# Kernel tuning notes

Measured on AMD Instinct MI355X. Metric: run time of the kernel, lower is better.

## Reference

```python
import jax, jax.numpy as jnp
import numpy as np

B, N, D, P = 8, 256, 1024, 512  # batch, n_words, input_dim, proj_dim


def setup_inputs() -> dict:
    key = jax.random.key(0)
    ks = jax.random.split(key, 8)
    w = lambda k, shape: (jax.random.normal(k, shape, dtype=jnp.float32) * 0.02)
    return {
        "x": jax.random.normal(ks[0], (B, N, D), dtype=jnp.float32),
        # bigram path
        "Wl": w(ks[1], (P, D)), "bl": jnp.zeros((P,), jnp.float32),
        "Wr": w(ks[2], (P, D)),  # right proj has no bias
        "Wo": w(ks[3], (1, P)), "bo": jnp.zeros((1,), jnp.float32),
        # start builder: Linear -> ReLU -> Linear
        "Ws1": w(ks[4], (P, D)), "bs1": jnp.zeros((P,), jnp.float32),
        "Ws2": w(ks[5], (1, P)), "bs2": jnp.zeros((1,), jnp.float32),
        # end builder
        "We1": w(ks[6], (P, D)), "be1": jnp.zeros((P,), jnp.float32),
        "We2": w(ks[7], (1, P)), "be2": jnp.zeros((1,), jnp.float32),
    }


def reference(x, Wl, bl, Wr, Wo, bo, Ws1, bs1, Ws2, bs2, We1, be1, We2, be2):
    # start / end scorers: [B,N,1]
    start = jax.nn.relu(jnp.einsum('bnd,pd->bnp', x, Ws1) + bs1) @ Ws2.T + bs2
    end = jax.nn.relu(jnp.einsum('bnd,pd->bnp', x, We1) + be1) @ We2.T + be2
    # bigram projections: [B,N,P]
    left = jnp.einsum('bnd,pd->bnp', x, Wl) + bl
    right = jnp.einsum('bnd,pd->bnp', x, Wr)
    # outer-sum: proj[b,i,j,:] = left[b,j,:] + right[b,i,:]  -> [B,N,N,P]
    proj = jax.nn.relu(left[:, None, :, :] + right[:, :, None, :])
    bigram = jnp.einsum('bijp,qp->bijq', proj, Wo) + bo  # [B,N,N,1]
    return (bigram, start, end)
```

## Files before the change

### kernel.cpp

```cpp
#include <hip/hip_runtime.h>

typedef __attribute__((ext_vector_type(8))) short short8;
typedef __attribute__((ext_vector_type(4))) float f32x4;

constexpr int kB = 8;
constexpr int kN = 256;
constexpr int kD = 1024;
constexpr int kP = 512;
constexpr int kM = kB * kN;

__global__ __launch_bounds__(256) void cvt_kernel(
    const float* __restrict__ x,
    const float* __restrict__ Wl, const float* __restrict__ Wr,
    const float* __restrict__ Ws1, const float* __restrict__ We1,
    unsigned short* __restrict__ xb, unsigned short* __restrict__ wb)
{
    const int g = blockIdx.x * 256 + threadIdx.x;
    const float* src;
    unsigned short* dst;
    if (g < 262144) {
        src = x + (size_t)g * 8;
        dst = xb + (size_t)g * 8;
    } else {
        const int gg = g - 262144;
        const int w = gg >> 16;
        const int r = gg & 65535;
        const float* s = (w == 0) ? Wl : (w == 1) ? Wr : (w == 2) ? Ws1 : We1;
        src = s + (size_t)r * 8;
        dst = wb + ((size_t)w << 19) + (size_t)r * 8;
    }
    const float4 a = *reinterpret_cast<const float4*>(src);
    const float4 b = *reinterpret_cast<const float4*>(src + 4);
    const float v[8] = {a.x, a.y, a.z, a.w, b.x, b.y, b.z, b.w};
    short8 o;
#pragma unroll
    for (int i = 0; i < 8; ++i) {
        unsigned u = __float_as_uint(v[i]);
        u = u + 0x7FFF + ((u >> 16) & 1);
        o[i] = (short)(u >> 16);
    }
    *reinterpret_cast<short8*>(dst) = o;
}

__global__ __launch_bounds__(256) void proj_mfma(
    const unsigned short* __restrict__ xb, const unsigned short* __restrict__ wb,
    const float* __restrict__ bl, const float* __restrict__ bs1,
    const float* __restrict__ be1,
    float* __restrict__ left_t, float* __restrict__ right_t,
    float* __restrict__ hs, float* __restrict__ he)
{
    const int z = blockIdx.z;
    const unsigned short* W = wb + ((size_t)z << 19);
    const float* bias = (z == 0) ? bl : (z == 2) ? bs1 : (z == 3) ? be1 : nullptr;
    float* dst = (z == 0) ? left_t : (z == 1) ? right_t : (z == 2) ? hs : he;
    const bool relu = (z >= 2);
    const bool transp = (z < 2);

    __shared__ unsigned short As[128 * 32];
    __shared__ unsigned short Bs[64 * 32];

    const int r0 = blockIdx.x * 128;
    const int p0 = blockIdx.y * 64;
    const int t = threadIdx.x;
    const int wid = t >> 6;
    const int lane = t & 63;
    const int wr = wid >> 1;
    const int wc = wid & 1;

    f32x4 acc[4][2] = {};

    const int lrow = lane >> 2;
    const int lcol = (lane & 3) * 8;
    const unsigned short* gA0 = xb + (size_t)(r0 + wid * 16 + lrow) * kD + lcol;
    const unsigned short* gA1 = gA0 + (size_t)64 * kD;
    const unsigned short* gB  = W  + (size_t)(p0 + wid * 16 + lrow) * kD + lcol;
    char* lA0 = (char*)As + wid * 1024;
    char* lA1 = (char*)As + 4096 + wid * 1024;
    char* lB  = (char*)Bs + wid * 1024;

    for (int k0 = 0; k0 < kD; k0 += 32) {
        __builtin_amdgcn_global_load_lds(
            (const __attribute__((address_space(1))) void*)(gA0 + k0),
            (__attribute__((address_space(3))) void*)lA0, 16, 0, 0);
        __builtin_amdgcn_global_load_lds(
            (const __attribute__((address_space(1))) void*)(gA1 + k0),
            (__attribute__((address_space(3))) void*)lA1, 16, 0, 0);
        __builtin_amdgcn_global_load_lds(
            (const __attribute__((address_space(1))) void*)(gB + k0),
            (__attribute__((address_space(3))) void*)lB, 16, 0, 0);
        __syncthreads();

        short8 a[4], b[2];
#pragma unroll
        for (int m = 0; m < 4; ++m)
            a[m] = *reinterpret_cast<const short8*>(
                &As[(wr * 64 + m * 16 + (lane & 15)) * 32 + (lane >> 4) * 8]);
#pragma unroll
        for (int n = 0; n < 2; ++n)
            b[n] = *reinterpret_cast<const short8*>(
                &Bs[(wc * 32 + n * 16 + (lane & 15)) * 32 + (lane >> 4) * 8]);
#pragma unroll
        for (int m = 0; m < 4; ++m)
#pragma unroll
            for (int n = 0; n < 2; ++n)
                acc[m][n] = __builtin_amdgcn_mfma_f32_16x16x32_bf16(
                    a[m], b[n], acc[m][n], 0, 0, 0);
        __syncthreads();
    }

    const int bb = r0 >> 8;
#pragma unroll
    for (int n = 0; n < 2; ++n) {
        const int p = p0 + wc * 32 + n * 16 + (lane & 15);
        const float bv = bias ? bias[p] : 0.f;
#pragma unroll
        for (int m = 0; m < 4; ++m) {
            const f32x4 c = acc[m][n];
            const int rbase = r0 + wr * 64 + m * 16 + (lane >> 4) * 4;
#pragma unroll
            for (int q = 0; q < 4; ++q) {
                float v = c[q] + bv;
                if (relu) v = fmaxf(v, 0.f);
                const int r = rbase + q;
                if (transp)
                    dst[((size_t)bb * kP + p) * kN + (r & 255)] = v;
                else
                    dst[(size_t)r * kP + p] = v;
            }
        }
    }
}

__global__ __launch_bounds__(256) void head_kernel(
    const float* __restrict__ hs, const float* __restrict__ Ws2,
    const float* __restrict__ bs2,
    const float* __restrict__ he, const float* __restrict__ We2,
    const float* __restrict__ be2,
    float* __restrict__ out_start, float* __restrict__ out_end)
{
    const int wave = threadIdx.x >> 6;
    const int lane = threadIdx.x & 63;
    const int r = blockIdx.x * 4 + wave;
    float ss = 0.f, ee = 0.f;
#pragma unroll
    for (int p = lane; p < kP; p += 64) {
        ss = fmaf(hs[(size_t)r * kP + p], Ws2[p], ss);
        ee = fmaf(he[(size_t)r * kP + p], We2[p], ee);
    }
#pragma unroll
    for (int off = 32; off > 0; off >>= 1) {
        ss += __shfl_down(ss, off);
        ee += __shfl_down(ee, off);
    }
    if (lane == 0) {
        out_start[r] = ss + bs2[0];
        out_end[r]   = ee + be2[0];
    }
}

__global__ __launch_bounds__(256) void bigram_kernel(
    const float* __restrict__ left_t, const float* __restrict__ right_t,
    const float* __restrict__ Wo, const float* __restrict__ bo,
    float* __restrict__ out)
{
    const int b  = blockIdx.z;
    const int i0 = blockIdx.y * 32;
    const int j0 = blockIdx.x * 64;

    __shared__ float ls[64][64];
    __shared__ float rs[64][32];
    __shared__ float wos[64];

    const int t  = threadIdx.x;
    const int tj = t & 15;
    const int ti = t >> 4;

    float acc[2][4] = {};

    const float* lb = left_t  + (size_t)b * kP * kN + j0;
    const float* rb = right_t + (size_t)b * kP * kN + i0;

    for (int pc = 0; pc < kP; pc += 64) {
#pragma unroll
        for (int h = 0; h < 4; ++h) {
            const int idx = h * 256 + t;
            const int pp = idx >> 4, jq = idx & 15;
            *reinterpret_cast<float4*>(&ls[pp][jq * 4]) =
                *reinterpret_cast<const float4*>(&lb[(size_t)(pc + pp) * kN + jq * 4]);
        }
#pragma unroll
        for (int h = 0; h < 2; ++h) {
            const int idx = h * 256 + t;
            const int pp = idx >> 3, iq = idx & 7;
            *reinterpret_cast<float4*>(&rs[pp][iq * 4]) =
                *reinterpret_cast<const float4*>(&rb[(size_t)(pc + pp) * kN + iq * 4]);
        }
        if (t < 64) wos[t] = Wo[pc + t];
        __syncthreads();

#pragma unroll 16
        for (int kk = 0; kk < 64; ++kk) {
            const float wo = wos[kk];
            const float4 lv = *reinterpret_cast<const float4*>(&ls[kk][tj * 4]);
            const float2 rv = *reinterpret_cast<const float2*>(&rs[kk][ti * 2]);
            const float lvv[4] = {lv.x, lv.y, lv.z, lv.w};
            const float rvv[2] = {rv.x, rv.y};
#pragma unroll
            for (int ii = 0; ii < 2; ++ii)
#pragma unroll
                for (int jj = 0; jj < 4; ++jj)
                    acc[ii][jj] = fmaf(fmaxf(rvv[ii] + lvv[jj], 0.f), wo, acc[ii][jj]);
        }
        __syncthreads();
    }

    const float bias = bo[0];
#pragma unroll
    for (int ii = 0; ii < 2; ++ii) {
        const int i = i0 + ti * 2 + ii;
        float4 o;
        o.x = acc[ii][0] + bias;
        o.y = acc[ii][1] + bias;
        o.z = acc[ii][2] + bias;
        o.w = acc[ii][3] + bias;
        *reinterpret_cast<float4*>(&out[((size_t)b * kN + i) * kN + j0 + tj * 4]) = o;
    }
}

extern "C" void kernel_launch(void* const* d_in, const int* in_sizes, int n_in,
                              void* d_out, int out_size, void* d_ws, size_t ws_size,
                              hipStream_t stream) {
    const float* x   = (const float*)d_in[0];
    const float* Wl  = (const float*)d_in[1];
    const float* bl  = (const float*)d_in[2];
    const float* Wr  = (const float*)d_in[3];
    const float* Wo  = (const float*)d_in[4];
    const float* bo  = (const float*)d_in[5];
    const float* Ws1 = (const float*)d_in[6];
    const float* bs1 = (const float*)d_in[7];
    const float* Ws2 = (const float*)d_in[8];
    const float* bs2 = (const float*)d_in[9];
    const float* We1 = (const float*)d_in[10];
    const float* be1 = (const float*)d_in[11];
    const float* We2 = (const float*)d_in[12];
    const float* be2 = (const float*)d_in[13];

    float* out        = (float*)d_out;
    float* out_bigram = out;
    float* out_start  = out + (size_t)kB * kN * kN;
    float* out_end    = out_start + (size_t)kB * kN;

    unsigned short* xb = (unsigned short*)d_ws;
    unsigned short* wb = xb + (size_t)2097152;
    float* left_t  = (float*)((char*)d_ws + (size_t)8 * 1024 * 1024);
    float* right_t = left_t  + (size_t)kM * kP;
    float* hs      = right_t + (size_t)kM * kP;
    float* he      = hs      + (size_t)kM * kP;

    cvt_kernel<<<2048, 256, 0, stream>>>(x, Wl, Wr, Ws1, We1, xb, wb);

    proj_mfma<<<dim3(kM / 128, kP / 64, 4), 256, 0, stream>>>(
        xb, wb, bl, bs1, be1, left_t, right_t, hs, he);

    head_kernel<<<kM / 4, 256, 0, stream>>>(
        hs, Ws2, bs2, he, We2, be2, out_start, out_end);

    bigram_kernel<<<dim3(kN / 64, kN / 32, kB), 256, 0, stream>>>(
        left_t, right_t, Wo, bo, out_bigram);
}
```

Measured before the change: 159.1 us.

## Move bigram to packed fp16, fuse start/end heads into GEMM epilogue, split-P reduce

The bigram outer-sum now runs in packed half2 arithmetic on fp16 left/right projections, split across eight P-chunks whose partial sums go to a separate reduce kernel. The start/end heads are fused into the projection GEMM epilogue through shuffle reductions and atomicAdd onto outputs pre-filled with the bias by the convert kernel, which removes the hs/he buffers and the head kernel. The GEMM also gains double-buffered LDS loads. Accumulating 64 terms in fp16 risks accuracy loss, and the float atomics make the start/end sums nondeterministic.

Result: faster. 138.1 us (-13.1%).

```diff
diff --git a/kernel.cpp b/kernel.cpp
--- a/kernel.cpp
+++ b/kernel.cpp
@@ -1,4 +1,5 @@
 #include <hip/hip_runtime.h>
+#include <hip/hip_fp16.h>
 
 typedef __attribute__((ext_vector_type(8))) short short8;
 typedef __attribute__((ext_vector_type(4))) float f32x4;
@@ -9,13 +10,30 @@
 constexpr int kP = 512;
 constexpr int kM = kB * kN;
 
+__device__ __forceinline__ __half2 pk_max2(__half2 a, __half2 b) {
+    unsigned ua = *reinterpret_cast<unsigned*>(&a);
+    unsigned ub = *reinterpret_cast<unsigned*>(&b);
+    unsigned ur;
+    asm("v_pk_max_f16 %0, %1, %2" : "=v"(ur) : "v"(ua), "v"(ub));
+    return *reinterpret_cast<__half2*>(&ur);
+}
+
 __global__ __launch_bounds__(256) void cvt_kernel(
     const float* __restrict__ x,
     const float* __restrict__ Wl, const float* __restrict__ Wr,
     const float* __restrict__ Ws1, const float* __restrict__ We1,
-    unsigned short* __restrict__ xb, unsigned short* __restrict__ wb)
+    const float* __restrict__ bs2, const float* __restrict__ be2,
+    unsigned short* __restrict__ xb, unsigned short* __restrict__ wb,
+    float* __restrict__ out_start, float* __restrict__ out_end)
 {
-    const int g = blockIdx.x * 256 + threadIdx.x;
+    const int bid = blockIdx.x;
+    if (bid >= 2048) {
+        const int idx = (bid - 2048) * 256 + threadIdx.x;
+        if (idx < 2048) out_start[idx] = bs2[0];
+        else            out_end[idx - 2048] = be2[0];
+        return;
+    }
+    const int g = bid * 256 + threadIdx.x;
     const float* src;
     unsigned short* dst;
     if (g < 262144) {
@@ -46,59 +64,52 @@
     const unsigned short* __restrict__ xb, const unsigned short* __restrict__ wb,
     const float* __restrict__ bl, const float* __restrict__ bs1,
     const float* __restrict__ be1,
-    float* __restrict__ left_t, float* __restrict__ right_t,
-    float* __restrict__ hs, float* __restrict__ he)
+    const float* __restrict__ Ws2, const float* __restrict__ We2,
+    __half* __restrict__ left_h, __half* __restrict__ right_h,
+    float* __restrict__ out_start, float* __restrict__ out_end)
 {
-    const int z = blockIdx.z;
-    const unsigned short* W = wb + ((size_t)z << 19);
-    const float* bias = (z == 0) ? bl : (z == 2) ? bs1 : (z == 3) ? be1 : nullptr;
-    float* dst = (z == 0) ? left_t : (z == 1) ? right_t : (z == 2) ? hs : he;
-    const bool relu = (z >= 2);
-    const bool transp = (z < 2);
-
-    __shared__ unsigned short As[128 * 32];
-    __shared__ unsigned short Bs[64 * 32];
+    __shared__ unsigned short As[2][128 * 32];
+    __shared__ unsigned short Bs[2][64 * 32];
 
     const int r0 = blockIdx.x * 128;
-    const int p0 = blockIdx.y * 64;
-    const int t = threadIdx.x;
-    const int wid = t >> 6;
-    const int lane = t & 63;
-    const int wr = wid >> 1;
-    const int wc = wid & 1;
+    const int q0 = blockIdx.y * 64;
+    const int z  = q0 >> 9;
+    const int t = threadIdx.x, wid = t >> 6, lane = t & 63;
+    const int wr = wid >> 1, wc = wid & 1;
 
     f32x4 acc[4][2] = {};
 
-    const int lrow = lane >> 2;
-    const int lcol = (lane & 3) * 8;
+    const int lrow = lane >> 2, lcol = (lane & 3) * 8;
     const unsigned short* gA0 = xb + (size_t)(r0 + wid * 16 + lrow) * kD + lcol;
     const unsigned short* gA1 = gA0 + (size_t)64 * kD;
-    const unsigned short* gB  = W  + (size_t)(p0 + wid * 16 + lrow) * kD + lcol;
-    char* lA0 = (char*)As + wid * 1024;
-    char* lA1 = (char*)As + 4096 + wid * 1024;
-    char* lB  = (char*)Bs + wid * 1024;
-
+    const unsigned short* gB  = wb + (size_t)(q0 + wid * 16 + lrow) * kD + lcol;
+
+#define STAGE(buf, k0) do { \
+    __builtin_amdgcn_global_load_lds( \
+        (const __attribute__((address_space(1))) void*)(gA0 + (k0)), \
+        (__attribute__((address_space(3))) void*)((char*)&As[buf][0] + wid * 1024), 16, 0, 0); \
+    __builtin_amdgcn_global_load_lds( \
+        (const __attribute__((address_space(1))) void*)(gA1 + (k0)), \
+        (__attribute__((address_space(3))) void*)((char*)&As[buf][0] + 4096 + wid * 1024), 16, 0, 0); \
+    __builtin_amdgcn_global_load_lds( \
+        (const __attribute__((address_space(1))) void*)(gB + (k0)), \
+        (__attribute__((address_space(3))) void*)((char*)&Bs[buf][0] + wid * 1024), 16, 0, 0); \
+} while (0)
+
+    STAGE(0, 0);
+    __syncthreads();
+    int cur = 0;
     for (int k0 = 0; k0 < kD; k0 += 32) {
-        __builtin_amdgcn_global_load_lds(
-            (const __attribute__((address_space(1))) void*)(gA0 + k0),
-            (__attribute__((address_space(3))) void*)lA0, 16, 0, 0);
-        __builtin_amdgcn_global_load_lds(
-            (const __attribute__((address_space(1))) void*)(gA1 + k0),
-            (__attribute__((address_space(3))) void*)lA1, 16, 0, 0);
-        __builtin_amdgcn_global_load_lds(
-            (const __attribute__((address_space(1))) void*)(gB + k0),
-            (__attribute__((address_space(3))) void*)lB, 16, 0, 0);
-        __syncthreads();
-
+        if (k0 + 32 < kD) STAGE(cur ^ 1, k0 + 32);
         short8 a[4], b[2];
 #pragma unroll
         for (int m = 0; m < 4; ++m)
             a[m] = *reinterpret_cast<const short8*>(
-                &As[(wr * 64 + m * 16 + (lane & 15)) * 32 + (lane >> 4) * 8]);
+                &As[cur][(wr * 64 + m * 16 + (lane & 15)) * 32 + (lane >> 4) * 8]);
 #pragma unroll
         for (int n = 0; n < 2; ++n)
             b[n] = *reinterpret_cast<const short8*>(
-                &Bs[(wc * 32 + n * 16 + (lane & 15)) * 32 + (lane >> 4) * 8]);
+                &Bs[cur][(wc * 32 + n * 16 + (lane & 15)) * 32 + (lane >> 4) * 8]);
 #pragma unroll
         for (int m = 0; m < 4; ++m)
 #pragma unroll
@@ -106,125 +117,150 @@
                 acc[m][n] = __builtin_amdgcn_mfma_f32_16x16x32_bf16(
                     a[m], b[n], acc[m][n], 0, 0, 0);
         __syncthreads();
-    }
-
-    const int bb = r0 >> 8;
+        cur ^= 1;
+    }
+#undef STAGE
+
+    int pcol[2]; float bq[2];
 #pragma unroll
     for (int n = 0; n < 2; ++n) {
-        const int p = p0 + wc * 32 + n * 16 + (lane & 15);
-        const float bv = bias ? bias[p] : 0.f;
-#pragma unroll
-        for (int m = 0; m < 4; ++m) {
-            const f32x4 c = acc[m][n];
-            const int rbase = r0 + wr * 64 + m * 16 + (lane >> 4) * 4;
-#pragma unroll
-            for (int q = 0; q < 4; ++q) {
-                float v = c[q] + bv;
-                if (relu) v = fmaxf(v, 0.f);
-                const int r = rbase + q;
-                if (transp)
-                    dst[((size_t)bb * kP + p) * kN + (r & 255)] = v;
-                else
-                    dst[(size_t)r * kP + p] = v;
+        pcol[n] = (q0 & 511) + wc * 32 + n * 16 + (lane & 15);
+        bq[n] = (z == 0) ? bl[pcol[n]] : (z == 2) ? bs1[pcol[n]]
+              : (z == 3) ? be1[pcol[n]] : 0.f;
+    }
+    if (z < 2) {
+        __half* dst = (z == 0) ? left_h : right_h;
+        const int bb = r0 >> 8;
+        const int jbase = (r0 & 255) + wr * 64 + (lane >> 4) * 4;
+#pragma unroll
+        for (int n = 0; n < 2; ++n) {
+            __half* drow = dst + (size_t)(bb * kP + pcol[n]) * kN;
+#pragma unroll
+            for (int m = 0; m < 4; ++m) {
+                const f32x4 c = acc[m][n];
+                __half2 h01 = __floats2half2_rn(c[0] + bq[n], c[1] + bq[n]);
+                __half2 h23 = __floats2half2_rn(c[2] + bq[n], c[3] + bq[n]);
+                uint2 u;
+                u.x = *reinterpret_cast<unsigned*>(&h01);
+                u.y = *reinterpret_cast<unsigned*>(&h23);
+                *reinterpret_cast<uint2*>(&drow[jbase + m * 16]) = u;
             }
         }
-    }
-}
-
-__global__ __launch_bounds__(256) void head_kernel(
-    const float* __restrict__ hs, const float* __restrict__ Ws2,
-    const float* __restrict__ bs2,
-    const float* __restrict__ he, const float* __restrict__ We2,
-    const float* __restrict__ be2,
-    float* __restrict__ out_start, float* __restrict__ out_end)
+    } else {
+        const float* Wv = (z == 2) ? Ws2 : We2;
+        float* outh = (z == 2) ? out_start : out_end;
+        const float w0 = Wv[pcol[0]], w1 = Wv[pcol[1]];
+        const int rbase = r0 + wr * 64 + (lane >> 4) * 4;
+#pragma unroll
+        for (int m = 0; m < 4; ++m) {
+#pragma unroll
+            for (int q = 0; q < 4; ++q) {
+                float s = fmaxf(acc[m][0][q] + bq[0], 0.f) * w0 +
+                          fmaxf(acc[m][1][q] + bq[1], 0.f) * w1;
+                s += __shfl_xor(s, 1); s += __shfl_xor(s, 2);
+                s += __shfl_xor(s, 4); s += __shfl_xor(s, 8);
+                if ((lane & 15) == 0)
+                    atomicAdd(&outh[rbase + m * 16 + q], s);
+            }
+        }
+    }
+}
+
+__global__ __launch_bounds__(256) void bigram_kernel(
+    const __half* __restrict__ left_h, const __half* __restrict__ right_h,
+    const float* __restrict__ Wo, float* __restrict__ part)
 {
-    const int wave = threadIdx.x >> 6;
-    const int lane = threadIdx.x & 63;
-    const int r = blockIdx.x * 4 + wave;
-    float ss = 0.f, ee = 0.f;
-#pragma unroll
-    for (int p = lane; p < kP; p += 64) {
-        ss = fmaf(hs[(size_t)r * kP + p], Ws2[p], ss);
-        ee = fmaf(he[(size_t)r * kP + p], We2[p], ee);
-    }
-#pragma unroll
-    for (int off = 32; off > 0; off >>= 1) {
-        ss += __shfl_down(ss, off);
-        ee += __shfl_down(ee, off);
-    }
-    if (lane == 0) {
-        out_start[r] = ss + bs2[0];
-        out_end[r]   = ee + be2[0];
-    }
-}
-
-__global__ __launch_bounds__(256) void bigram_kernel(
-    const float* __restrict__ left_t, const float* __restrict__ right_t,
-    const float* __restrict__ Wo, const float* __restrict__ bo,
+    __shared__ __half ls[64][64];
+    __shared__ __half2 rs2[64][64];
+    __shared__ __half2 wos[64];
+
+    const int bz = blockIdx.z, b = bz >> 3, pc = bz & 7;
+    const int i0 = blockIdx.y * 64, j0 = blockIdx.x * 64;
+    const int t = threadIdx.x, wid = t >> 6, lane = t & 63;
+    const int tj = t & 15, ti = t >> 4;
+
+    const __half* lbase = left_h  + (size_t)(b * kP + pc * 64) * kN;
+    const __half* rbase = right_h + (size_t)(b * kP + pc * 64) * kN;
+
+#pragma unroll
+    for (int h = 0; h < 2; ++h) {
+        const int row = wid * 16 + h * 8 + (lane >> 3);
+        __builtin_amdgcn_global_load_lds(
+            (const __attribute__((address_space(1))) void*)
+                (lbase + (size_t)row * kN + j0 + (lane & 7) * 8),
+            (__attribute__((address_space(3))) void*)
+                ((char*)&ls[0][0] + wid * 2048 + h * 1024),
+            16, 0, 0);
+    }
+    uint2 rload[4];
+#pragma unroll
+    for (int h = 0; h < 4; ++h) {
+        const int idx = h * 256 + t, pp = idx >> 4, iq = idx & 15;
+        rload[h] = *reinterpret_cast<const uint2*>(&rbase[(size_t)pp * kN + i0 + iq * 4]);
+    }
+    if (t < 64) wos[t] = __float2half2_rn(Wo[pc * 64 + t]);
+#pragma unroll
+    for (int h = 0; h < 4; ++h) {
+        const int idx = h * 256 + t, pp = idx >> 4, iq = idx & 15;
+        const unsigned lo = rload[h].x, hi = rload[h].y;
+        uint4 d;
+        d.x = (lo & 0xFFFFu) | (lo << 16);
+        d.y = (lo >> 16)     | (lo & 0xFFFF0000u);
+        d.z = (hi & 0xFFFFu) | (hi << 16);
+        d.w = (hi >> 16)     | (hi & 0xFFFF0000u);
+        *reinterpret_cast<uint4*>(&rs2[pp][iq * 4]) = d;
+    }
+    __syncthreads();
+
+    const __half2 zero2 = __float2half2_rn(0.f);
+    __half2 acc2[4][2];
+#pragma unroll
+    for (int ii = 0; ii < 4; ++ii)
+#pragma unroll
+        for (int jp = 0; jp < 2; ++jp) acc2[ii][jp] = zero2;
+
+#pragma unroll 8
+    for (int kk = 0; kk < 64; ++kk) {
+        const __half2 wo2 = wos[kk];
+        union { uint2 u; __half2 h[2]; } L;
+        L.u = *reinterpret_cast<const uint2*>(&ls[kk][tj * 4]);
+        union { uint4 u; __half2 h[4]; } R;
+        R.u = *reinterpret_cast<const uint4*>(&rs2[kk][ti * 4]);
+#pragma unroll
+        for (int ii = 0; ii < 4; ++ii)
+#pragma unroll
+            for (int jp = 0; jp < 2; ++jp) {
+                __half2 s = __hadd2(R.h[ii], L.h[jp]);
+                s = pk_max2(s, zero2);
+                acc2[ii][jp] = __hfma2(s, wo2, acc2[ii][jp]);
+            }
+    }
+
+    float* po = part + (size_t)bz * 65536;
+#pragma unroll
+    for (int ii = 0; ii < 4; ++ii) {
+        const float2 a = __half22float2(acc2[ii][0]);
+        const float2 c = __half22float2(acc2[ii][1]);
+        float4 o = {a.x, a.y, c.x, c.y};
+        *reinterpret_cast<float4*>(&po[(i0 + ti * 4 + ii) * kN + j0 + tj * 4]) = o;
+    }
+}
+
+__global__ __launch_bounds__(256) void reduce_kernel(
+    const float* __restrict__ part, const float* __restrict__ bo,
     float* __restrict__ out)
 {
-    const int b  = blockIdx.z;
-    const int i0 = blockIdx.y * 32;
-    const int j0 = blockIdx.x * 64;
-
-    __shared__ float ls[64][64];
-    __shared__ float rs[64][32];
-    __shared__ float wos[64];
-
-    const int t  = threadIdx.x;
-    const int tj = t & 15;
-    const int ti = t >> 4;
-
-    float acc[2][4] = {};
-
-    const float* lb = left_t  + (size_t)b * kP * kN + j0;
-    const float* rb = right_t + (size_t)b * kP * kN + i0;
-
-    for (int pc = 0; pc < kP; pc += 64) {
-#pragma unroll
-        for (int h = 0; h < 4; ++h) {
-            const int idx = h * 256 + t;
-            const int pp = idx >> 4, jq = idx & 15;
-            *reinterpret_cast<float4*>(&ls[pp][jq * 4]) =
-                *reinterpret_cast<const float4*>(&lb[(size_t)(pc + pp) * kN + jq * 4]);
-        }
-#pragma unroll
-        for (int h = 0; h < 2; ++h) {
-            const int idx = h * 256 + t;
-            const int pp = idx >> 3, iq = idx & 7;
-            *reinterpret_cast<float4*>(&rs[pp][iq * 4]) =
-                *reinterpret_cast<const float4*>(&rb[(size_t)(pc + pp) * kN + iq * 4]);
-        }
-        if (t < 64) wos[t] = Wo[pc + t];
-        __syncthreads();
-
-#pragma unroll 16
-        for (int kk = 0; kk < 64; ++kk) {
-            const float wo = wos[kk];
-            const float4 lv = *reinterpret_cast<const float4*>(&ls[kk][tj * 4]);
-            const float2 rv = *reinterpret_cast<const float2*>(&rs[kk][ti * 2]);
-            const float lvv[4] = {lv.x, lv.y, lv.z, lv.w};
-            const float rvv[2] = {rv.x, rv.y};
-#pragma unroll
-            for (int ii = 0; ii < 2; ++ii)
-#pragma unroll
-                for (int jj = 0; jj < 4; ++jj)
-                    acc[ii][jj] = fmaf(fmaxf(rvv[ii] + lvv[jj], 0.f), wo, acc[ii][jj]);
-        }
-        __syncthreads();
-    }
-
+    const int e4 = blockIdx.x * 256 + threadIdx.x;
+    const int e = e4 * 4, b = e >> 16, r = e & 65535;
     const float bias = bo[0];
-#pragma unroll
-    for (int ii = 0; ii < 2; ++ii) {
-        const int i = i0 + ti * 2 + ii;
-        float4 o;
-        o.x = acc[ii][0] + bias;
-        o.y = acc[ii][1] + bias;
-        o.z = acc[ii][2] + bias;
-        o.w = acc[ii][3] + bias;
-        *reinterpret_cast<float4*>(&out[((size_t)b * kN + i) * kN + j0 + tj * 4]) = o;
-    }
+    float4 acc = {bias, bias, bias, bias};
+#pragma unroll
+    for (int k = 0; k < 8; ++k) {
+        const float4 v = *reinterpret_cast<const float4*>(
+            &part[(size_t)(b * 8 + k) * 65536 + r]);
+        acc.x += v.x; acc.y += v.y; acc.z += v.z; acc.w += v.w;
+    }
+    *reinterpret_cast<float4*>(&out[e]) = acc;
 }
 
 extern "C" void kernel_launch(void* const* d_in, const int* in_sizes, int n_in,
@@ -250,21 +286,20 @@
     float* out_start  = out + (size_t)kB * kN * kN;
     float* out_end    = out_start + (size_t)kB * kN;
 
-    unsigned short* xb = (unsigned short*)d_ws;
+    __half* left_h  = (__half*)d_ws;
+    __half* right_h = left_h + (size_t)1048576;
+    unsigned short* xb = (unsigned short*)((char*)d_ws + (size_t)4 * 1024 * 1024);
     unsigned short* wb = xb + (size_t)2097152;
-    float* left_t  = (float*)((char*)d_ws + (size_t)8 * 1024 * 1024);
-    float* right_t = left_t  + (size_t)kM * kP;
-    float* hs      = right_t + (size_t)kM * kP;
-    float* he      = hs      + (size_t)kM * kP;
-
-    cvt_kernel<<<2048, 256, 0, stream>>>(x, Wl, Wr, Ws1, We1, xb, wb);
-
-    proj_mfma<<<dim3(kM / 128, kP / 64, 4), 256, 0, stream>>>(
-        xb, wb, bl, bs1, be1, left_t, right_t, hs, he);
-
-    head_kernel<<<kM / 4, 256, 0, stream>>>(
-        hs, Ws2, bs2, he, We2, be2, out_start, out_end);
-
-    bigram_kernel<<<dim3(kN / 64, kN / 32, kB), 256, 0, stream>>>(
-        left_t, right_t, Wo, bo, out_bigram);
-}
+    float* part = (float*)((char*)d_ws + (size_t)4 * 1024 * 1024);
+
+    cvt_kernel<<<2064, 256, 0, stream>>>(
+        x, Wl, Wr, Ws1, We1, bs2, be2, xb, wb, out_start, out_end);
+
+    proj_mfma<<<dim3(16, 32), 256, 0, stream>>>(
+        xb, wb, bl, bs1, be1, Ws2, We2, left_h, right_h, out_start, out_end);
+
+    bigram_kernel<<<dim3(4, 4, 64), 256, 0, stream>>>(
+        left_h, right_h, Wo, part);
+
+    reduce_kernel<<<512, 256, 0, stream>>>(part, bo, out_bigram);
+}
```
